# Kernel optimization log

Measured on AMD Instinct MI355X. Metric: run time of the kernel, lower is better.

The kernel has to match this reference:

```python
import jax, jax.numpy as jnp
import numpy as np

B, S, D, H, L, F, V = 8, 4096, 1024, 16, 6, 2048, 256
DH = D // H

def _pe(seq, dim):
    pos = jnp.arange(seq, dtype=jnp.float32)[:, None]
    div = jnp.exp(jnp.arange(0, dim, 2, dtype=jnp.float32) * (-np.log(10000.0) / dim))
    pe = jnp.zeros((seq, dim), jnp.float32)
    pe = pe.at[:, 0::2].set(jnp.sin(pos * div))
    pe = pe.at[:, 1::2].set(jnp.cos(pos * div))
    return pe

def _ln(x, w, b):
    m = x.mean(-1, keepdims=True)
    v = ((x - m) ** 2).mean(-1, keepdims=True)
    return (x - m) * jax.lax.rsqrt(v + 1e-5) * w + b

def setup_inputs():
    key = jax.random.key(0)
    ks = jax.random.split(key, 8)
    s = 0.02
    return {
        'tgt': jax.random.normal(ks[0], (B, S, D), jnp.float32),
        'in_proj_w': jax.random.normal(ks[1], (L, 3 * D, D), jnp.float32) * s,
        'in_proj_b': jnp.zeros((L, 3 * D), jnp.float32),
        'out_proj_w': jax.random.normal(ks[2], (L, D, D), jnp.float32) * s,
        'out_proj_b': jnp.zeros((L, D), jnp.float32),
        'ln1_w': jnp.ones((L, D), jnp.float32), 'ln1_b': jnp.zeros((L, D), jnp.float32),
        'lin1_w': jax.random.normal(ks[3], (L, F, D), jnp.float32) * s,
        'lin1_b': jnp.zeros((L, F), jnp.float32),
        'lin2_w': jax.random.normal(ks[4], (L, D, F), jnp.float32) * s,
        'lin2_b': jnp.zeros((L, D), jnp.float32),
        'ln2_w': jnp.ones((L, D), jnp.float32), 'ln2_b': jnp.zeros((L, D), jnp.float32),
        'w_out': jax.random.normal(ks[5], (V, D), jnp.float32) * s,
        'b_out': jnp.zeros((V,), jnp.float32),
    }

def reference(tgt, in_proj_w, in_proj_b, out_proj_w, out_proj_b, ln1_w, ln1_b,
              lin1_w, lin1_b, lin2_w, lin2_b, ln2_w, ln2_b, w_out, b_out):
    # eval-mode cached decode step of CachedDecoderOnly.forward (dropout inactive)
    out = tgt + _pe(S, D)[None]  # [B,S,D]
    for i in range(L):
        q = out[:, -1:, :]  # query is only the last token
        wq, wk, wv = jnp.split(in_proj_w[i], 3, axis=0)
        bq, bk, bv = jnp.split(in_proj_b[i], 3)
        Q = (q @ wq.T + bq).reshape(B, 1, H, DH)
        K = (out @ wk.T + bk).reshape(B, -1, H, DH)
        Vv = (out @ wv.T + bv).reshape(B, -1, H, DH)
        sc = jnp.einsum('bqhd,bkhd->bhqk', Q, K) / jnp.sqrt(jnp.float32(DH))
        a = jax.nn.softmax(sc, axis=-1)
        o = jnp.einsum('bhqk,bkhd->bqhd', a, Vv).reshape(B, 1, D)
        o = o @ out_proj_w[i].T + out_proj_b[i]
        y = _ln(q + o, ln1_w[i], ln1_b[i])
        ff = jax.nn.relu(y @ lin1_w[i].T + lin1_b[i]) @ lin2_w[i].T + lin2_b[i]
        out = _ln(y + ff, ln2_w[i], ln2_b[i])  # [B,1,D] -> src for next layer
    return out @ w_out.T + b_out  # [B,1,V]
```

## Files before the change

kernel.cpp:

```cpp
#include <hip/hip_runtime.h>
#include <hip/hip_bf16.h>

#define BB 8
#define SS 4096
#define DD 1024
#define HH 16
#define LL 6
#define FF 2048
#define VV 256
#define NCS 8

typedef __attribute__((ext_vector_type(8))) short bf16x8;
typedef __attribute__((ext_vector_type(4))) float f32x4;

__device__ __forceinline__ unsigned short f2bf(float f) {
    union { float f; unsigned u; } v; v.f = f;
    unsigned r = v.u + 0x7FFFu + ((v.u >> 16) & 1u);
    return (unsigned short)(r >> 16);
}

__global__ __launch_bounds__(256) void pe_kernel(float* __restrict__ pe) {
    int s = blockIdx.x;
    float fs = (float)s;
    for (int i = threadIdx.x; i < DD / 2; i += 256) {
        float div = expf((-logf(10000.0f) / (float)DD) * (float)(2 * i));
        float a = fs * div;
        pe[(long)s * DD + 2 * i]     = sinf(a);
        pe[(long)s * DD + 2 * i + 1] = cosf(a);
    }
}

template <int K, int RELU, int MODE>
__global__ __launch_bounds__(256) void gemm8k(
    const float* __restrict__ A, long sA,
    const float* __restrict__ A2, long sA2,
    const float* __restrict__ W,
    const float* __restrict__ bias,
    const float* __restrict__ R1, long sR1,
    const float* __restrict__ R2, long sR2,
    const float* __restrict__ lnw, const float* __restrict__ lnb,
    const float* __restrict__ lnsrc,
    float* __restrict__ C, int N)
{
    int wave = threadIdx.x >> 6, lane = threadIdx.x & 63;
    int n = blockIdx.x * 4 + wave;
    if (n >= N) return;

    float mean[8], rstd[8];
    if (MODE != 0) {
        const float* S = (MODE == 1) ? A : lnsrc;
        long ss = (MODE == 1) ? sA : 1024L;
        const int SK = (MODE == 1) ? K : 1024;
        #pragma unroll
        for (int m = 0; m < 8; ++m) {
            float s1 = 0.f, s2 = 0.f;
            const float4* Sr = reinterpret_cast<const float4*>(S + (long)m * ss);
            #pragma unroll
            for (int k4 = 0; k4 < SK / 256; ++k4) {
                float4 a = Sr[k4 * 64 + lane];
                s1 += a.x + a.y + a.z + a.w;
                s2 += a.x * a.x + a.y * a.y + a.z * a.z + a.w * a.w;
            }
            for (int off = 32; off; off >>= 1) {
                s1 += __shfl_xor(s1, off, 64);
                s2 += __shfl_xor(s2, off, 64);
            }
            float mu = s1 / (float)SK;
            mean[m] = mu;
            rstd[m] = rsqrtf(s2 / (float)SK - mu * mu + 1e-5f);
        }
    }

    float acc[8] = {0.f,0.f,0.f,0.f,0.f,0.f,0.f,0.f};
    const float4* W4 = reinterpret_cast<const float4*>(W + (long)n * K);
    float4 wv[K / 256];
    #pragma unroll
    for (int kb = 0; kb < K / 256; ++kb) wv[kb] = W4[kb * 64 + lane];
    #pragma unroll
    for (int kb = 0; kb < K / 256; ++kb) {
        int k4 = kb * 64 + lane;
        float4 w = wv[kb];
        float4 lw, lb;
        if (MODE == 1) {
            lw = reinterpret_cast<const float4*>(lnw)[k4];
            lb = reinterpret_cast<const float4*>(lnb)[k4];
        }
        #pragma unroll
        for (int m = 0; m < 8; ++m) {
            float4 a = reinterpret_cast<const float4*>(A + (long)m * sA)[k4];
            if (A2) {
                float4 a2 = reinterpret_cast<const float4*>(A2 + (long)m * sA2)[k4];
                a.x += a2.x; a.y += a2.y; a.z += a2.z; a.w += a2.w;
            }
            if (MODE == 1) {
                float mu = mean[m], rs = rstd[m];
                a.x = (a.x - mu) * rs * lw.x + lb.x;
                a.y = (a.y - mu) * rs * lw.y + lb.y;
                a.z = (a.z - mu) * rs * lw.z + lb.z;
                a.w = (a.w - mu) * rs * lw.w + lb.w;
            }
            acc[m] += a.x * w.x + a.y * w.y + a.z * w.z + a.w * w.w;
        }
    }
    #pragma unroll
    for (int m = 0; m < 8; ++m)
        for (int off = 32; off; off >>= 1) acc[m] += __shfl_xor(acc[m], off, 64);
    if (lane == 0) {
        float bs = bias ? bias[n] : 0.f;
        #pragma unroll
        for (int m = 0; m < 8; ++m) {
            float v = acc[m] + bs;
            if (MODE == 0) {
                if (R1) v += R1[(long)m * sR1 + n];
                if (R2) v += R2[(long)m * sR2 + n];
            }
            if (MODE == 2)
                v += (lnsrc[(long)m * 1024 + n] - mean[m]) * rstd[m] * lnw[n] + lnb[n];
            if (RELU) v = fmaxf(v, 0.f);
            C[(long)m * N + n] = v;
        }
    }
}

__global__ __launch_bounds__(256) void u_kernel(const float* __restrict__ Q,
                                                const float* __restrict__ wk,
                                                unsigned short* __restrict__ ub)
{
    int h = blockIdx.y;
    int e = blockIdx.x * 256 + threadIdx.x;
    __shared__ float qs[8][64];
    for (int idx = threadIdx.x; idx < 512; idx += 256) {
        int b = idx >> 6, d = idx & 63;
        qs[b][d] = Q[(long)b * DD + h * 64 + d];
    }
    __syncthreads();
    float acc[8] = {0.f,0.f,0.f,0.f,0.f,0.f,0.f,0.f};
    for (int d = 0; d < 64; ++d) {
        float wv = wk[(long)(h * 64 + d) * DD + e];
        #pragma unroll
        for (int b = 0; b < 8; ++b) acc[b] += qs[b][d] * wv;
    }
    #pragma unroll
    for (int b = 0; b < 8; ++b)
        ub[((long)(b * HH + h)) * DD + e] = f2bf(acc[b]);
}

__global__ __launch_bounds__(256) void score_kernel(const float* __restrict__ tgt,
                                                    const float* __restrict__ pe,
                                                    const unsigned short* __restrict__ ub,
                                                    float* __restrict__ scp)
{
    int b = blockIdx.z, h2 = blockIdx.y;
    int wave = threadIdx.x >> 6, lane = threadIdx.x & 63;
    int q = lane >> 4, n = lane & 15;
    int s = blockIdx.x * 64 + wave * 16 + n;
    f32x4 acc = {0.f, 0.f, 0.f, 0.f};
    const float* xrow = tgt + ((long)b * SS + s) * DD;
    const float* prow = pe + (long)s * DD;
    const unsigned short* urow = ub + ((long)(b * HH) + n) * DD;
    #pragma unroll 4
    for (int ks = 0; ks < 16; ++ks) {
        int e0 = h2 * 512 + ks * 32 + q * 8;
        bf16x8 a = *reinterpret_cast<const bf16x8*>(urow + e0);
        float4 x0 = *reinterpret_cast<const float4*>(xrow + e0);
        float4 x1 = *reinterpret_cast<const float4*>(xrow + e0 + 4);
        float4 p0 = *reinterpret_cast<const float4*>(prow + e0);
        float4 p1 = *reinterpret_cast<const float4*>(prow + e0 + 4);
        union { short sh[8]; bf16x8 v; } bu;
        bu.sh[0] = (short)f2bf(x0.x + p0.x);
        bu.sh[1] = (short)f2bf(x0.y + p0.y);
        bu.sh[2] = (short)f2bf(x0.z + p0.z);
        bu.sh[3] = (short)f2bf(x0.w + p0.w);
        bu.sh[4] = (short)f2bf(x1.x + p1.x);
        bu.sh[5] = (short)f2bf(x1.y + p1.y);
        bu.sh[6] = (short)f2bf(x1.z + p1.z);
        bu.sh[7] = (short)f2bf(x1.w + p1.w);
        acc = __builtin_amdgcn_mfma_f32_16x16x32_bf16(a, bu.v, acc, 0, 0, 0);
    }
    #pragma unroll
    for (int r = 0; r < 4; ++r) {
        int h = q * 4 + r;
        scp[(((long)h2 * BB + b) * HH + h) * SS + s] = acc[r];
    }
}

__global__ __launch_bounds__(256) void softmax_kernel(const float* __restrict__ scp,
                                                      unsigned int* __restrict__ pb)
{
    int row = blockIdx.x;
    int t = threadIdx.x;
    const float4* p0 = reinterpret_cast<const float4*>(scp + (long)row * SS);
    const float4* p1 = reinterpret_cast<const float4*>(scp + ((long)BB * HH + row) * SS);
    float4 v[4];
    float mx = -3.0e38f;
    #pragma unroll
    for (int i = 0; i < 4; ++i) {
        float4 a = p0[t + 256 * i], c = p1[t + 256 * i];
        v[i] = make_float4((a.x + c.x) * 0.125f, (a.y + c.y) * 0.125f,
                           (a.z + c.z) * 0.125f, (a.w + c.w) * 0.125f);
        mx = fmaxf(mx, fmaxf(fmaxf(v[i].x, v[i].y), fmaxf(v[i].z, v[i].w)));
    }
    __shared__ float red[4];
    for (int off = 32; off; off >>= 1) mx = fmaxf(mx, __shfl_xor(mx, off, 64));
    if ((t & 63) == 0) red[t >> 6] = mx;
    __syncthreads();
    mx = fmaxf(fmaxf(red[0], red[1]), fmaxf(red[2], red[3]));
    __syncthreads();
    float sum = 0.f;
    #pragma unroll
    for (int i = 0; i < 4; ++i) {
        v[i].x = expf(v[i].x - mx); v[i].y = expf(v[i].y - mx);
        v[i].z = expf(v[i].z - mx); v[i].w = expf(v[i].w - mx);
        sum += v[i].x + v[i].y + v[i].z + v[i].w;
    }
    for (int off = 32; off; off >>= 1) sum += __shfl_xor(sum, off, 64);
    if ((t & 63) == 0) red[t >> 6] = sum;
    __syncthreads();
    sum = red[0] + red[1] + red[2] + red[3];
    float inv = 1.f / sum;
    #pragma unroll
    for (int i = 0; i < 4; ++i) {
        unsigned d0 = (unsigned)f2bf(v[i].x * inv) | ((unsigned)f2bf(v[i].y * inv) << 16);
        unsigned d1 = (unsigned)f2bf(v[i].z * inv) | ((unsigned)f2bf(v[i].w * inv) << 16);
        reinterpret_cast<uint2*>(pb)[(long)row * 1024 + t + 256 * i] = make_uint2(d0, d1);
    }
}

__global__ __launch_bounds__(256) void ctx_kernel(const float* __restrict__ tgt,
                                                  const float* __restrict__ pe,
                                                  const unsigned short* __restrict__ pb,
                                                  float* __restrict__ ctxp)
{
    int b = blockIdx.z, sc = blockIdx.y, et = blockIdx.x;
    int wave = threadIdx.x >> 6, lane = threadIdx.x & 63;
    int q = lane >> 4, n = lane & 15;
    int e = et * 64 + wave * 16 + n;
    f32x4 acc = {0.f, 0.f, 0.f, 0.f};
    const unsigned short* prow = pb + ((long)(b * HH) + n) * SS;
    #pragma unroll 2
    for (int ks = 0; ks < 16; ++ks) {
        int sb = sc * 512 + ks * 32 + q * 8;
        bf16x8 a = *reinterpret_cast<const bf16x8*>(prow + sb);
        union { short sh[8]; bf16x8 v; } bu;
        #pragma unroll
        for (int j = 0; j < 8; ++j) {
            float xv = tgt[((long)b * SS + sb + j) * DD + e] + pe[(long)(sb + j) * DD + e];
            bu.sh[j] = (short)f2bf(xv);
        }
        acc = __builtin_amdgcn_mfma_f32_16x16x32_bf16(a, bu.v, acc, 0, 0, 0);
    }
    #pragma unroll
    for (int r = 0; r < 4; ++r)
        ctxp[(((long)sc * BB + b) * HH + q * 4 + r) * DD + e] = acc[r];
}

__global__ __launch_bounds__(256) void ctxred_kernel(const float* __restrict__ ctxp,
                                                     float* __restrict__ ctx)
{
    long i = ((long)blockIdx.x * 256 + threadIdx.x) * 4;
    float4 s = make_float4(0.f, 0.f, 0.f, 0.f);
    #pragma unroll
    for (int c = 0; c < NCS; ++c) {
        float4 p = *reinterpret_cast<const float4*>(ctxp + (long)c * BB * HH * DD + i);
        s.x += p.x; s.y += p.y; s.z += p.z; s.w += p.w;
    }
    *reinterpret_cast<float4*>(ctx + i) = s;
}

__global__ __launch_bounds__(256) void ov_kernel(const float* __restrict__ ctx,
                                                 const float* __restrict__ wv,
                                                 const float* __restrict__ bv,
                                                 float* __restrict__ o)
{
    int wave = threadIdx.x >> 6, lane = threadIdx.x & 63;
    int j = blockIdx.x * 4 + wave;
    if (j >= DD) return;
    int h = j >> 6;
    float acc[8] = {0.f,0.f,0.f,0.f,0.f,0.f,0.f,0.f};
    const float4* w4 = reinterpret_cast<const float4*>(wv + (long)j * DD);
    float4 wreg[4];
    #pragma unroll
    for (int kb = 0; kb < 4; ++kb) wreg[kb] = w4[kb * 64 + lane];
    #pragma unroll
    for (int kb = 0; kb < 4; ++kb) {
        int k4 = kb * 64 + lane;
        float4 w = wreg[kb];
        #pragma unroll
        for (int b = 0; b < 8; ++b) {
            float4 a = reinterpret_cast<const float4*>(ctx + ((long)(b * HH + h)) * DD)[k4];
            acc[b] += a.x * w.x + a.y * w.y + a.z * w.z + a.w * w.w;
        }
    }
    #pragma unroll
    for (int b = 0; b < 8; ++b)
        for (int off = 32; off; off >>= 1) acc[b] += __shfl_xor(acc[b], off, 64);
    if (lane == 0) {
        float bs = bv[j];
        #pragma unroll
        for (int b = 0; b < 8; ++b) o[(long)b * DD + j] = acc[b] + bs;
    }
}

extern "C" void kernel_launch(void* const* d_in, const int* in_sizes, int n_in,
                              void* d_out, int out_size, void* d_ws, size_t ws_size,
                              hipStream_t stream)
{
    const float* tgt        = (const float*)d_in[0];
    const float* in_proj_w  = (const float*)d_in[1];
    const float* in_proj_b  = (const float*)d_in[2];
    const float* out_proj_w = (const float*)d_in[3];
    const float* out_proj_b = (const float*)d_in[4];
    const float* ln1_w      = (const float*)d_in[5];
    const float* ln1_b      = (const float*)d_in[6];
    const float* lin1_w     = (const float*)d_in[7];
    const float* lin1_b     = (const float*)d_in[8];
    const float* lin2_w     = (const float*)d_in[9];
    const float* lin2_b     = (const float*)d_in[10];
    const float* ln2_w      = (const float*)d_in[11];
    const float* ln2_b      = (const float*)d_in[12];
    const float* w_out      = (const float*)d_in[13];
    const float* b_out      = (const float*)d_in[14];

    float* ws = (float*)d_ws;
    long off = 0;
    float* pe   = ws + off;  off += (long)SS * DD;
    float* scp  = ws + off;  off += 2L * BB * HH * SS;
    float* ctxp = ws + off;  off += (long)NCS * BB * HH * DD;
    float* ctx  = ws + off;  off += (long)BB * HH * DD;
    unsigned short* pb = (unsigned short*)(ws + off); off += (long)BB * HH * SS / 2;
    unsigned short* ub = (unsigned short*)(ws + off); off += (long)BB * HH * DD / 2;
    float* Q    = ws + off;  off += (long)BB * DD;
    float* o    = ws + off;  off += (long)BB * DD;
    float* vb   = ws + off;  off += (long)BB * DD;
    float* o2   = ws + off;  off += (long)BB * DD;
    float* hb   = ws + off;  off += (long)BB * FF;
    float* z    = ws + off;  off += (long)BB * DD;

    const float* tgt_last = tgt + (long)(SS - 1) * DD;
    const float* pe_last  = pe + (long)(SS - 1) * DD;

    pe_kernel<<<SS, 256, 0, stream>>>(pe);

    gemm8k<1024, 0, 0><<<DD / 4, 256, 0, stream>>>(
        tgt_last, (long)SS * DD, pe_last, 0L, in_proj_w, in_proj_b,
        nullptr, 0L, nullptr, 0L, nullptr, nullptr, nullptr, Q, DD);

    u_kernel<<<dim3(4, 16), 256, 0, stream>>>(Q, in_proj_w + (long)DD * DD, ub);

    score_kernel<<<dim3(SS / 64, 2, BB), 256, 0, stream>>>(tgt, pe, ub, scp);
    softmax_kernel<<<BB * HH, 256, 0, stream>>>(scp, (unsigned int*)pb);
    ctx_kernel<<<dim3(DD / 64, NCS, BB), 256, 0, stream>>>(tgt, pe, pb, ctxp);
    ctxred_kernel<<<(BB * HH * DD) / 1024, 256, 0, stream>>>(ctxp, ctx);

    ov_kernel<<<DD / 4, 256, 0, stream>>>(ctx, in_proj_w + 2L * DD * DD, in_proj_b + 2 * DD, o);

    gemm8k<1024, 0, 0><<<DD / 4, 256, 0, stream>>>(
        o, (long)DD, nullptr, 0L, out_proj_w, out_proj_b,
        tgt_last, (long)SS * DD, pe_last, 0L, nullptr, nullptr, nullptr, o2, DD);
    gemm8k<1024, 1, 1><<<FF / 4, 256, 0, stream>>>(
        o2, (long)DD, nullptr, 0L, lin1_w, lin1_b,
        nullptr, 0L, nullptr, 0L, ln1_w, ln1_b, nullptr, hb, FF);
    gemm8k<2048, 0, 2><<<DD / 4, 256, 0, stream>>>(
        hb, (long)FF, nullptr, 0L, lin2_w, lin2_b,
        nullptr, 0L, nullptr, 0L, ln1_w, ln1_b, o2, z, DD);

    for (int i = 1; i < LL; ++i) {
        const float* wv_i  = in_proj_w + (long)i * 3 * DD * DD + 2L * DD * DD;
        const float* bv_i  = in_proj_b + (long)i * 3 * DD + 2 * DD;
        const float* l2w_p = ln2_w + (long)(i - 1) * DD;
        const float* l2b_p = ln2_b + (long)(i - 1) * DD;
        const float* l1w   = ln1_w + (long)i * DD;
        const float* l1b   = ln1_b + (long)i * DD;
        gemm8k<1024, 0, 1><<<DD / 4, 256, 0, stream>>>(
            z, (long)DD, nullptr, 0L, wv_i, bv_i,
            nullptr, 0L, nullptr, 0L, l2w_p, l2b_p, nullptr, vb, DD);
        gemm8k<1024, 0, 2><<<DD / 4, 256, 0, stream>>>(
            vb, (long)DD, nullptr, 0L,
            out_proj_w + (long)i * DD * DD, out_proj_b + (long)i * DD,
            nullptr, 0L, nullptr, 0L, l2w_p, l2b_p, z, o2, DD);
        gemm8k<1024, 1, 1><<<FF / 4, 256, 0, stream>>>(
            o2, (long)DD, nullptr, 0L,
            lin1_w + (long)i * FF * DD, lin1_b + (long)i * FF,
            nullptr, 0L, nullptr, 0L, l1w, l1b, nullptr, hb, FF);
        gemm8k<2048, 0, 2><<<DD / 4, 256, 0, stream>>>(
            hb, (long)FF, nullptr, 0L,
            lin2_w + (long)i * DD * FF, lin2_b + (long)i * DD,
            nullptr, 0L, nullptr, 0L, l1w, l1b, o2, z, DD);
    }

    gemm8k<1024, 0, 1><<<VV / 4, 256, 0, stream>>>(
        z, (long)DD, nullptr, 0L, w_out, b_out,
        nullptr, 0L, nullptr, 0L,
        ln2_w + (long)(LL - 1) * DD, ln2_b + (long)(LL - 1) * DD, nullptr,
        (float*)d_out, VV);
}
```

Baseline: 615.0 us.

## Fuse score, softmax and context into a split-sequence flash-decoding attention kernel

Replaces the separate score, softmax and context kernels with one attention kernel. Each block handles a 128-token chunk for one batch: it computes the scores with MFMA, does a local softmax in LDS, and multiplies the unnormalised probabilities by the values. A reduction kernel then rescales and merges the 32 chunk partials using their max and sum statistics. This removes the round trips of the full score and probability arrays through global memory and cuts the number of launches. In exchange the grid has only 256 large blocks, the activations are still read twice per block, and there are more partial context buffers to merge.

```diff
diff --git a/kernel.cpp b/kernel.cpp
--- a/kernel.cpp
+++ b/kernel.cpp
@@ -8,7 +8,7 @@
 #define LL 6
 #define FF 2048
 #define VV 256
-#define NCS 8
+#define NC 32
 
 typedef __attribute__((ext_vector_type(8))) short bf16x8;
 typedef __attribute__((ext_vector_type(4))) float f32x4;
@@ -145,126 +145,134 @@
         ub[((long)(b * HH + h)) * DD + e] = f2bf(acc[b]);
 }
 
-__global__ __launch_bounds__(256) void score_kernel(const float* __restrict__ tgt,
-                                                    const float* __restrict__ pe,
-                                                    const unsigned short* __restrict__ ub,
-                                                    float* __restrict__ scp)
-{
-    int b = blockIdx.z, h2 = blockIdx.y;
+__global__ __launch_bounds__(512) void attn_kernel(
+    const float* __restrict__ tgt, const float* __restrict__ pe,
+    const unsigned short* __restrict__ ub,
+    float* __restrict__ ctxp, float* __restrict__ ml)
+{
+    int sc = blockIdx.x, b = blockIdx.y;
     int wave = threadIdx.x >> 6, lane = threadIdx.x & 63;
     int q = lane >> 4, n = lane & 15;
-    int s = blockIdx.x * 64 + wave * 16 + n;
-    f32x4 acc = {0.f, 0.f, 0.f, 0.f};
-    const float* xrow = tgt + ((long)b * SS + s) * DD;
-    const float* prow = pe + (long)s * DD;
-    const unsigned short* urow = ub + ((long)(b * HH) + n) * DD;
-    #pragma unroll 4
-    for (int ks = 0; ks < 16; ++ks) {
-        int e0 = h2 * 512 + ks * 32 + q * 8;
-        bf16x8 a = *reinterpret_cast<const bf16x8*>(urow + e0);
-        float4 x0 = *reinterpret_cast<const float4*>(xrow + e0);
-        float4 x1 = *reinterpret_cast<const float4*>(xrow + e0 + 4);
-        float4 p0 = *reinterpret_cast<const float4*>(prow + e0);
-        float4 p1 = *reinterpret_cast<const float4*>(prow + e0 + 4);
-        union { short sh[8]; bf16x8 v; } bu;
-        bu.sh[0] = (short)f2bf(x0.x + p0.x);
-        bu.sh[1] = (short)f2bf(x0.y + p0.y);
-        bu.sh[2] = (short)f2bf(x0.z + p0.z);
-        bu.sh[3] = (short)f2bf(x0.w + p0.w);
-        bu.sh[4] = (short)f2bf(x1.x + p1.x);
-        bu.sh[5] = (short)f2bf(x1.y + p1.y);
-        bu.sh[6] = (short)f2bf(x1.z + p1.z);
-        bu.sh[7] = (short)f2bf(x1.w + p1.w);
-        acc = __builtin_amdgcn_mfma_f32_16x16x32_bf16(a, bu.v, acc, 0, 0, 0);
-    }
-    #pragma unroll
-    for (int r = 0; r < 4; ++r) {
-        int h = q * 4 + r;
-        scp[(((long)h2 * BB + b) * HH + h) * SS + s] = acc[r];
-    }
-}
-
-__global__ __launch_bounds__(256) void softmax_kernel(const float* __restrict__ scp,
-                                                      unsigned int* __restrict__ pb)
+    __shared__ float scs[16][128];
+    __shared__ unsigned short P[16 * 128];
+
+    int s0 = sc * 128;
+
+    {
+        int s = s0 + wave * 16 + n;
+        const float* xrow = tgt + ((long)b * SS + s) * DD;
+        const float* prow = pe + (long)s * DD;
+        const unsigned short* urow = ub + ((long)(b * HH) + n) * DD;
+        f32x4 acc = {0.f, 0.f, 0.f, 0.f};
+        #pragma unroll 4
+        for (int ks = 0; ks < 32; ++ks) {
+            int e0 = ks * 32 + q * 8;
+            bf16x8 a = *reinterpret_cast<const bf16x8*>(urow + e0);
+            float4 x0 = *reinterpret_cast<const float4*>(xrow + e0);
+            float4 x1 = *reinterpret_cast<const float4*>(xrow + e0 + 4);
+            float4 p0 = *reinterpret_cast<const float4*>(prow + e0);
+            float4 p1 = *reinterpret_cast<const float4*>(prow + e0 + 4);
+            union { short sh[8]; bf16x8 v; } bu;
+            bu.sh[0] = (short)f2bf(x0.x + p0.x);
+            bu.sh[1] = (short)f2bf(x0.y + p0.y);
+            bu.sh[2] = (short)f2bf(x0.z + p0.z);
+            bu.sh[3] = (short)f2bf(x0.w + p0.w);
+            bu.sh[4] = (short)f2bf(x1.x + p1.x);
+            bu.sh[5] = (short)f2bf(x1.y + p1.y);
+            bu.sh[6] = (short)f2bf(x1.z + p1.z);
+            bu.sh[7] = (short)f2bf(x1.w + p1.w);
+            acc = __builtin_amdgcn_mfma_f32_16x16x32_bf16(a, bu.v, acc, 0, 0, 0);
+        }
+        #pragma unroll
+        for (int r = 0; r < 4; ++r) scs[q * 4 + r][wave * 16 + n] = acc[r];
+    }
+    __syncthreads();
+
+    {
+        int h = threadIdx.x >> 5, l = threadIdx.x & 31;
+        float4 v = *reinterpret_cast<const float4*>(&scs[h][l * 4]);
+        v.x *= 0.125f; v.y *= 0.125f; v.z *= 0.125f; v.w *= 0.125f;
+        float mx = fmaxf(fmaxf(v.x, v.y), fmaxf(v.z, v.w));
+        #pragma unroll
+        for (int off = 16; off; off >>= 1) mx = fmaxf(mx, __shfl_xor(mx, off, 32));
+        float e0 = expf(v.x - mx), e1 = expf(v.y - mx);
+        float e2 = expf(v.z - mx), e3 = expf(v.w - mx);
+        float sum = e0 + e1 + e2 + e3;
+        #pragma unroll
+        for (int off = 16; off; off >>= 1) sum += __shfl_xor(sum, off, 32);
+        unsigned d0 = (unsigned)f2bf(e0) | ((unsigned)f2bf(e1) << 16);
+        unsigned d1 = (unsigned)f2bf(e2) | ((unsigned)f2bf(e3) << 16);
+        char* Pb = reinterpret_cast<char*>(P);
+        *reinterpret_cast<uint2*>(Pb + ((h * 256 + l * 8) ^ ((h & 7) << 4))) = make_uint2(d0, d1);
+        if (l == 0) {
+            long mi = ((long)sc * BB + b) * HH + h;
+            ml[mi * 2] = mx;
+            ml[mi * 2 + 1] = sum;
+        }
+    }
+    __syncthreads();
+
+    {
+        const char* Pb = reinterpret_cast<const char*>(P);
+        f32x4 cacc[8];
+        #pragma unroll
+        for (int t = 0; t < 8; ++t) cacc[t] = (f32x4){0.f, 0.f, 0.f, 0.f};
+        #pragma unroll
+        for (int ks2 = 0; ks2 < 4; ++ks2) {
+            int sb = ks2 * 32 + q * 8;
+            bf16x8 a = *reinterpret_cast<const bf16x8*>(
+                Pb + ((n * 256 + sb * 2) ^ ((n & 7) << 4)));
+            const float* xb  = tgt + ((long)b * SS + s0 + sb) * DD;
+            const float* pb2 = pe + (long)(s0 + sb) * DD;
+            #pragma unroll
+            for (int t = 0; t < 8; ++t) {
+                int e = wave * 128 + t * 16 + n;
+                union { short sh[8]; bf16x8 v; } bu;
+                #pragma unroll
+                for (int j = 0; j < 8; ++j)
+                    bu.sh[j] = (short)f2bf(xb[(long)j * DD + e] + pb2[(long)j * DD + e]);
+                cacc[t] = __builtin_amdgcn_mfma_f32_16x16x32_bf16(a, bu.v, cacc[t], 0, 0, 0);
+            }
+        }
+        long base = (((long)sc * BB + b) * HH) * DD;
+        #pragma unroll
+        for (int t = 0; t < 8; ++t) {
+            int e = wave * 128 + t * 16 + n;
+            #pragma unroll
+            for (int r = 0; r < 4; ++r)
+                ctxp[base + (long)(q * 4 + r) * DD + e] = cacc[t][r];
+        }
+    }
+}
+
+__global__ __launch_bounds__(256) void ctxred_kernel(const float* __restrict__ ctxp,
+                                                     const float* __restrict__ ml,
+                                                     float* __restrict__ ctx)
 {
     int row = blockIdx.x;
-    int t = threadIdx.x;
-    const float4* p0 = reinterpret_cast<const float4*>(scp + (long)row * SS);
-    const float4* p1 = reinterpret_cast<const float4*>(scp + ((long)BB * HH + row) * SS);
-    float4 v[4];
-    float mx = -3.0e38f;
-    #pragma unroll
-    for (int i = 0; i < 4; ++i) {
-        float4 a = p0[t + 256 * i], c = p1[t + 256 * i];
-        v[i] = make_float4((a.x + c.x) * 0.125f, (a.y + c.y) * 0.125f,
-                           (a.z + c.z) * 0.125f, (a.w + c.w) * 0.125f);
-        mx = fmaxf(mx, fmaxf(fmaxf(v[i].x, v[i].y), fmaxf(v[i].z, v[i].w)));
-    }
-    __shared__ float red[4];
-    for (int off = 32; off; off >>= 1) mx = fmaxf(mx, __shfl_xor(mx, off, 64));
-    if ((t & 63) == 0) red[t >> 6] = mx;
-    __syncthreads();
-    mx = fmaxf(fmaxf(red[0], red[1]), fmaxf(red[2], red[3]));
-    __syncthreads();
-    float sum = 0.f;
-    #pragma unroll
-    for (int i = 0; i < 4; ++i) {
-        v[i].x = expf(v[i].x - mx); v[i].y = expf(v[i].y - mx);
-        v[i].z = expf(v[i].z - mx); v[i].w = expf(v[i].w - mx);
-        sum += v[i].x + v[i].y + v[i].z + v[i].w;
-    }
-    for (int off = 32; off; off >>= 1) sum += __shfl_xor(sum, off, 64);
-    if ((t & 63) == 0) red[t >> 6] = sum;
-    __syncthreads();
-    sum = red[0] + red[1] + red[2] + red[3];
-    float inv = 1.f / sum;
-    #pragma unroll
-    for (int i = 0; i < 4; ++i) {
-        unsigned d0 = (unsigned)f2bf(v[i].x * inv) | ((unsigned)f2bf(v[i].y * inv) << 16);
-        unsigned d1 = (unsigned)f2bf(v[i].z * inv) | ((unsigned)f2bf(v[i].w * inv) << 16);
-        reinterpret_cast<uint2*>(pb)[(long)row * 1024 + t + 256 * i] = make_uint2(d0, d1);
-    }
-}
-
-__global__ __launch_bounds__(256) void ctx_kernel(const float* __restrict__ tgt,
-                                                  const float* __restrict__ pe,
-                                                  const unsigned short* __restrict__ pb,
-                                                  float* __restrict__ ctxp)
-{
-    int b = blockIdx.z, sc = blockIdx.y, et = blockIdx.x;
-    int wave = threadIdx.x >> 6, lane = threadIdx.x & 63;
-    int q = lane >> 4, n = lane & 15;
-    int e = et * 64 + wave * 16 + n;
-    f32x4 acc = {0.f, 0.f, 0.f, 0.f};
-    const unsigned short* prow = pb + ((long)(b * HH) + n) * SS;
-    #pragma unroll 2
-    for (int ks = 0; ks < 16; ++ks) {
-        int sb = sc * 512 + ks * 32 + q * 8;
-        bf16x8 a = *reinterpret_cast<const bf16x8*>(prow + sb);
-        union { short sh[8]; bf16x8 v; } bu;
-        #pragma unroll
-        for (int j = 0; j < 8; ++j) {
-            float xv = tgt[((long)b * SS + sb + j) * DD + e] + pe[(long)(sb + j) * DD + e];
-            bu.sh[j] = (short)f2bf(xv);
-        }
-        acc = __builtin_amdgcn_mfma_f32_16x16x32_bf16(a, bu.v, acc, 0, 0, 0);
-    }
-    #pragma unroll
-    for (int r = 0; r < 4; ++r)
-        ctxp[(((long)sc * BB + b) * HH + q * 4 + r) * DD + e] = acc[r];
-}
-
-__global__ __launch_bounds__(256) void ctxred_kernel(const float* __restrict__ ctxp,
-                                                     float* __restrict__ ctx)
-{
-    long i = ((long)blockIdx.x * 256 + threadIdx.x) * 4;
+    float M = -3.0e38f;
+    #pragma unroll
+    for (int c = 0; c < NC; ++c) M = fmaxf(M, ml[((long)c * BB * HH + row) * 2]);
+    float L = 0.f;
+    float scl[NC];
+    #pragma unroll
+    for (int c = 0; c < NC; ++c) {
+        float e = expf(ml[((long)c * BB * HH + row) * 2] - M);
+        scl[c] = e;
+        L += e * ml[((long)c * BB * HH + row) * 2 + 1];
+    }
+    float inv = 1.f / L;
+    int e4 = threadIdx.x * 4;
     float4 s = make_float4(0.f, 0.f, 0.f, 0.f);
     #pragma unroll
-    for (int c = 0; c < NCS; ++c) {
-        float4 p = *reinterpret_cast<const float4*>(ctxp + (long)c * BB * HH * DD + i);
-        s.x += p.x; s.y += p.y; s.z += p.z; s.w += p.w;
-    }
-    *reinterpret_cast<float4*>(ctx + i) = s;
+    for (int c = 0; c < NC; ++c) {
+        float4 p = *reinterpret_cast<const float4*>(
+            ctxp + ((long)c * BB * HH + row) * DD + e4);
+        float f = scl[c];
+        s.x += p.x * f; s.y += p.y * f; s.z += p.z * f; s.w += p.w * f;
+    }
+    s.x *= inv; s.y *= inv; s.z *= inv; s.w *= inv;
+    *reinterpret_cast<float4*>(ctx + (long)row * DD + e4) = s;
 }
 
 __global__ __launch_bounds__(256) void ov_kernel(const float* __restrict__ ctx,
@@ -324,10 +332,9 @@
     float* ws = (float*)d_ws;
     long off = 0;
     float* pe   = ws + off;  off += (long)SS * DD;
-    float* scp  = ws + off;  off += 2L * BB * HH * SS;
-    float* ctxp = ws + off;  off += (long)NCS * BB * HH * DD;
+    float* ctxp = ws + off;  off += (long)NC * BB * HH * DD;
+    float* ml   = ws + off;  off += (long)NC * BB * HH * 2;
     float* ctx  = ws + off;  off += (long)BB * HH * DD;
-    unsigned short* pb = (unsigned short*)(ws + off); off += (long)BB * HH * SS / 2;
     unsigned short* ub = (unsigned short*)(ws + off); off += (long)BB * HH * DD / 2;
     float* Q    = ws + off;  off += (long)BB * DD;
     float* o    = ws + off;  off += (long)BB * DD;
@@ -347,10 +354,8 @@
 
     u_kernel<<<dim3(4, 16), 256, 0, stream>>>(Q, in_proj_w + (long)DD * DD, ub);
 
-    score_kernel<<<dim3(SS / 64, 2, BB), 256, 0, stream>>>(tgt, pe, ub, scp);
-    softmax_kernel<<<BB * HH, 256, 0, stream>>>(scp, (unsigned int*)pb);
-    ctx_kernel<<<dim3(DD / 64, NCS, BB), 256, 0, stream>>>(tgt, pe, pb, ctxp);
-    ctxred_kernel<<<(BB * HH * DD) / 1024, 256, 0, stream>>>(ctxp, ctx);
+    attn_kernel<<<dim3(NC, BB), 512, 0, stream>>>(tgt, pe, ub, ctxp, ml);
+    ctxred_kernel<<<BB * HH, 256, 0, stream>>>(ctxp, ml, ctx);
 
     ov_kernel<<<DD / 4, 256, 0, stream>>>(ctx, in_proj_w + 2L * DD * DD, in_proj_b + 2 * DD, o);
 
```

Result: no change. 614.6 us (-0.1%).
